# Performance work log

Hardware: AMD Instinct MI355X
Metric: run time of the kernel (lower is better)

## Reference

```python
import jax, jax.numpy as jnp
import numpy as np
import math

B, TD, TP, D, H = 16, 256, 1024, 512, 8
DH = D // H
G_MIN = 0.05
LN_EPS = 1e-5
SCALE = 1.0 / math.sqrt(DH)


def _ln(x, g, b):
    m = jnp.mean(x, axis=-1, keepdims=True)
    v = jnp.var(x, axis=-1, keepdims=True)
    return (x - m) * jax.lax.rsqrt(v + LN_EPS) * g + b


def _evi(x, w1, b1, w2, b2, k):
    # EvidentialHead: Linear -> SiLU -> Linear(d->4), NIG params -> gate
    h = jax.nn.silu(x @ w1 + b1)
    p = h @ w2 + b2  # (B,T,4)
    gamma, nu, alpha, beta = jnp.split(p, 4, axis=-1)
    nu = jax.nn.softplus(nu) + 1e-6
    alpha = jax.nn.softplus(alpha) + 1.0
    beta = jax.nn.softplus(beta) + 1e-6
    sigma2 = beta / (nu * (alpha - 1.0))  # (B,T,1)
    g = jnp.clip(jnp.exp(-k * sigma2[..., 0]), G_MIN, 1.0)  # (B,T)
    return g


def _xattn(Q, KV, log_bias, wq, bq, wk, bk, wv, bv, wo, bo, lng, lnb):
    # Q: (B,M,D), KV: (B,N,D), log_bias: (B,N) added to logits pre-softmax
    Bq, M, _ = Q.shape
    N = KV.shape[1]
    q = (Q @ wq + bq).reshape(Bq, M, H, DH)
    k_ = (KV @ wk + bk).reshape(Bq, N, H, DH)
    v = (KV @ wv + bv).reshape(Bq, N, H, DH)
    scores = jnp.einsum('bmhd,bnhd->bhmn', q, k_) * SCALE
    scores = scores + log_bias[:, None, None, :]
    attn = jax.nn.softmax(scores, axis=-1)
    out = jnp.einsum('bhmn,bnhd->bmhd', attn, v).reshape(Bq, M, D)
    out = out @ wo + bo
    return _ln(Q + out, lng, lnb)


def _ffn(x, w1, b1, w2, b2, lng, lnb):
    # Linear(d,4d) -> SiLU -> Linear(4d,d) -> LayerNorm (no residual)
    h = jax.nn.silu(x @ w1 + b1)
    return _ln(h @ w2 + b2, lng, lnb)


def setup_inputs() -> dict:
    key = jax.random.key(0)
    ks = iter(jax.random.split(key, 64))

    def w(shape, s=0.02):
        return s * jax.random.normal(next(ks), shape, jnp.float32)

    def attn_params(pfx):
        p = {}
        for nm in ('wq', 'wk', 'wv', 'wo'):
            p[pfx + '_' + nm] = w((D, D))
        for nm in ('bq', 'bk', 'bv', 'bo'):
            p[pfx + '_' + nm] = jnp.zeros((D,), jnp.float32)
        p[pfx + '_lng'] = jnp.ones((D,), jnp.float32)
        p[pfx + '_lnb'] = jnp.zeros((D,), jnp.float32)
        return p

    def ffn_params(pfx):
        return {pfx + '_w1': w((D, 4 * D)), pfx + '_b1': jnp.zeros((4 * D,), jnp.float32),
                pfx + '_w2': w((4 * D, D)), pfx + '_b2': jnp.zeros((D,), jnp.float32),
                pfx + '_lng': jnp.ones((D,), jnp.float32), pfx + '_lnb': jnp.zeros((D,), jnp.float32)}

    inp = {
        'Hd': jax.random.normal(next(ks), (B, TD, D), jnp.float32),
        'Hp': jax.random.normal(next(ks), (B, TP, D), jnp.float32),
        'k': 1,
        'evid_w1': w((D, D)), 'evid_b1': jnp.zeros((D,), jnp.float32),
        'evid_w2': w((D, 4)), 'evid_b2': jnp.zeros((4,), jnp.float32),
        'evip_w1': w((D, D)), 'evip_b1': jnp.zeros((D,), jnp.float32),
        'evip_w2': w((D, 4)), 'evip_b2': jnp.zeros((4,), jnp.float32),
    }
    inp.update(attn_params('p2d'))
    inp.update(attn_params('d2p'))
    inp.update(ffn_params('ffnd'))
    inp.update(ffn_params('ffnp'))
    return inp


def reference(Hd, Hp, k,
              evid_w1, evid_b1, evid_w2, evid_b2,
              evip_w1, evip_b1, evip_w2, evip_b2,
              p2d_wq, p2d_wk, p2d_wv, p2d_wo, p2d_bq, p2d_bk, p2d_bv, p2d_bo, p2d_lng, p2d_lnb,
              d2p_wq, d2p_wk, d2p_wv, d2p_wo, d2p_bq, d2p_bk, d2p_bv, d2p_bo, d2p_lng, d2p_lnb,
              ffnd_w1, ffnd_b1, ffnd_w2, ffnd_b2, ffnd_lng, ffnd_lnb,
              ffnp_w1, ffnp_b1, ffnp_w2, ffnp_b2, ffnp_lng, ffnp_lnb):
    gd = _evi(Hd, evid_w1, evid_b1, evid_w2, evid_b2, k)  # (B,TD)
    gp = _evi(Hp, evip_w1, evip_b1, evip_w2, evip_b2, k)  # (B,TP)
    Hp2 = _xattn(Hp, Hd, jnp.log(gd + 1e-12),
                 p2d_wq, p2d_bq, p2d_wk, p2d_bk, p2d_wv, p2d_bv, p2d_wo, p2d_bo, p2d_lng, p2d_lnb)
    Hd2 = _xattn(Hd, Hp, jnp.log(gp + 1e-12),
                 d2p_wq, d2p_bq, d2p_wk, d2p_bk, d2p_wv, d2p_bv, d2p_wo, d2p_bo, d2p_lng, d2p_lnb)
    Hd_out = _ffn(Hd2, ffnd_w1, ffnd_b1, ffnd_w2, ffnd_b2, ffnd_lng, ffnd_lnb)
    Hp_out = _ffn(Hp2, ffnp_w1, ffnp_b1, ffnp_w2, ffnp_b2, ffnp_lng, ffnp_lnb)
    return (Hd_out, Hp_out, gd, gp)
```

## Files before the change

kernel.cpp:

```cpp
#include <hip/hip_runtime.h>
#include <stdint.h>
#include <math.h>

typedef unsigned short u16;
typedef __attribute__((ext_vector_type(8))) short bf16x8;
typedef __attribute__((ext_vector_type(8))) short short8;
typedef __attribute__((ext_vector_type(4))) float f32x4;
typedef __attribute__((ext_vector_type(4))) unsigned short u16x4;

#define NB 16
#define TDr 256
#define TPr 1024
#define DM 512
#define NH 8
#define DHEAD 64

__device__ __forceinline__ float us2f(u16 u) {
  union { float f; unsigned int i; } x; x.i = ((unsigned int)u) << 16; return x.f;
}
__device__ __forceinline__ u16 f2us(float f) {
  union { float fl; unsigned int i; } x; x.fl = f;
  unsigned int u = x.i;
  return (u16)((u + 0x7fffu + ((u >> 16) & 1u)) >> 16);
}

__global__ __launch_bounds__(64) void detect_kernel(const u16* __restrict__ raw,
                                                    int* __restrict__ flag)
{
  const int lane = threadIdx.x;
  float mx = 0.f;
  for (int i = lane; i < 256; i += 64) {
    float v = us2f(raw[i]);
    v = fabsf(v);
    if (isfinite(v)) mx = fmaxf(mx, v); else mx = 1e30f;
  }
#pragma unroll
  for (int o = 32; o; o >>= 1) mx = fmaxf(mx, __shfl_xor(mx, o));
  if (lane == 0) flag[0] = (mx > 1e10f) ? 1 : 0;
}

struct CvtDesc { const void* src; unsigned long dst_off; int n; };
struct CvtTable { CvtDesc d[42]; };

__global__ __launch_bounds__(256) void cvt_kernel(CvtTable t, u16* __restrict__ base,
                                                  const int* __restrict__ flag)
{
  const CvtDesc d = t.d[blockIdx.y];
  u16* dst = base + d.dst_off;
  const int isf32 = flag[0];
  const int stride = gridDim.x * 256;
  const int tid0 = blockIdx.x * 256 + threadIdx.x;
  if (d.n >= 8) {
    const int n8 = d.n >> 3;
    if (isf32) {
      const float* s = (const float*)d.src;
      for (int i = tid0; i < n8; i += stride) {
        f32x4 a = *(const f32x4*)&s[i * 8];
        f32x4 b = *(const f32x4*)&s[i * 8 + 4];
        short8 o;
        o[0]=(short)f2us(a[0]); o[1]=(short)f2us(a[1]); o[2]=(short)f2us(a[2]); o[3]=(short)f2us(a[3]);
        o[4]=(short)f2us(b[0]); o[5]=(short)f2us(b[1]); o[6]=(short)f2us(b[2]); o[7]=(short)f2us(b[3]);
        *(short8*)&dst[i * 8] = o;
      }
    } else {
      const short8* s = (const short8*)d.src;
      for (int i = tid0; i < n8; i += stride) *(short8*)&dst[i * 8] = s[i];
    }
  } else {
    if (isf32) {
      const float* s = (const float*)d.src;
      for (int i = tid0; i < d.n; i += stride) dst[i] = f2us(s[i]);
    } else {
      const u16* s = (const u16*)d.src;
      for (int i = tid0; i < d.n; i += stride) dst[i] = s[i];
    }
  }
}

template<int BM, int BN>
__device__ __forceinline__ void gemm_core(
    const u16* __restrict__ Ab, const u16* __restrict__ Bb,
    int K, int tid, f32x4 (&acc)[BM/32][BN/32])
{
  constexpr int BK = 32;
  constexpr int FM = BM / 32;
  constexpr int FN = BN / 32;
  constexpr int LPT = (BM * BK / 8 + BN * BK / 8) / 256;
  __shared__ __align__(16) u16 As[2][BM * BK];
  __shared__ __align__(16) u16 Bs[2][BN * BK];

  const int lane = tid & 63;
  const int wm = (tid >> 6) >> 1;
  const int wn = (tid >> 6) & 1;

#pragma unroll
  for (int i = 0; i < FM; ++i)
#pragma unroll
    for (int j = 0; j < FN; ++j)
      acc[i][j] = (f32x4){0.f, 0.f, 0.f, 0.f};

  auto stage = [&](int buf, int k0) {
#pragma unroll
    for (int c = tid; c < BM * BK / 8; c += 256) {
      const int r  = c >> 2;
      const int kk = (c & 3) << 3;
      __builtin_amdgcn_global_load_lds(
          (const __attribute__((address_space(1))) uint32_t*)(Ab + (long)r * K + k0 + kk),
          (__attribute__((address_space(3))) uint32_t*)(&As[buf][c * 8]), 16, 0, 0);
    }
#pragma unroll
    for (int c = tid; c < BN * BK / 8; c += 256) {
      const int r  = c >> 2;
      const int kk = (c & 3) << 3;
      __builtin_amdgcn_global_load_lds(
          (const __attribute__((address_space(1))) uint32_t*)(Bb + (long)r * K + k0 + kk),
          (__attribute__((address_space(3))) uint32_t*)(&Bs[buf][c * 8]), 16, 0, 0);
    }
  };

  const int nt = K / BK;
  stage(0, 0);
  if (nt > 1) stage(1, BK);

  for (int t = 0; t < nt; ++t) {
    if (t + 1 < nt) {
      if constexpr (LPT == 4) asm volatile("s_waitcnt vmcnt(4)" ::: "memory");
      else                    asm volatile("s_waitcnt vmcnt(3)" ::: "memory");
    } else {
      asm volatile("s_waitcnt vmcnt(0)" ::: "memory");
    }
    asm volatile("s_barrier" ::: "memory");
    __builtin_amdgcn_sched_barrier(0);

    const int cur = t & 1;
    bf16x8 af[FM], bfv[FN];
#pragma unroll
    for (int i = 0; i < FM; ++i)
      af[i] = *(const bf16x8*)&As[cur][(wm * (BM/2) + i*16 + (lane & 15)) * BK + ((lane >> 4) << 3)];
#pragma unroll
    for (int j = 0; j < FN; ++j)
      bfv[j] = *(const bf16x8*)&Bs[cur][(wn * (BN/2) + j*16 + (lane & 15)) * BK + ((lane >> 4) << 3)];
#pragma unroll
    for (int i = 0; i < FM; ++i)
#pragma unroll
      for (int j = 0; j < FN; ++j)
        acc[i][j] = __builtin_amdgcn_mfma_f32_16x16x32_bf16(af[i], bfv[j], acc[i][j], 0, 0, 0);

    __builtin_amdgcn_sched_barrier(0);
    asm volatile("s_barrier" ::: "memory");
    __builtin_amdgcn_sched_barrier(0);
    if (t + 2 < nt) stage(cur, (t + 2) * BK);
  }
}

struct ProjSet {
  const u16 *A, *W, *bE, *bQ, *bK, *bV;
  u16 *H, *Q, *Kc, *VT;
  int ntokLog, mtiles;
};

__global__ __launch_bounds__(256, 4) void proj_pair(ProjSet s0, ProjSet s1)
{
  const ProjSet S = blockIdx.z ? s1 : s0;
  if ((int)blockIdx.x >= S.mtiles) return;
  const int tid = threadIdx.x;
  const int lane = tid & 63;
  const int wm = (tid >> 6) >> 1, wn = (tid >> 6) & 1;
  const int r16 = lane & 15, rr4 = (lane >> 4) << 2;
  const long row0 = (long)blockIdx.x * 128;
  const long col0 = (long)blockIdx.y * 128;

  f32x4 acc[4][4];
  gemm_core<128,128>(S.A + row0 * 512, S.W + col0 * 512, 512, tid, acc);

  const int range = (int)(col0 >> 9);
  const u16* bp = range == 0 ? S.bE : range == 1 ? S.bQ : range == 2 ? S.bK : S.bV;
  u16* dst = range == 0 ? S.H : range == 1 ? S.Q : S.Kc;
  const int ntok = 1 << S.ntokLog;

#pragma unroll
  for (int i = 0; i < 4; ++i) {
    const long gr0 = row0 + wm*64 + i*16 + rr4;
#pragma unroll
    for (int j = 0; j < 4; ++j) {
      const int cr = (int)(col0 & 511) + wn*64 + j*16 + r16;
      const float badd = us2f(bp[cr]);
      if (range == 3) {
        const long b = gr0 >> S.ntokLog;
        const long t0 = gr0 & (ntok - 1);
        u16x4 pk;
#pragma unroll
        for (int r = 0; r < 4; ++r) pk[r] = f2us(acc[i][j][r] + badd);
        *(u16x4*)&S.VT[((long)b * 512 + cr) * ntok + t0] = pk;
      } else if (range == 0) {
#pragma unroll
        for (int r = 0; r < 4; ++r) {
          float v = acc[i][j][r] + badd;
          v = v / (1.f + __expf(-v));
          dst[(gr0 + r) * 512 + cr] = f2us(v);
        }
      } else {
#pragma unroll
        for (int r = 0; r < 4; ++r)
          dst[(gr0 + r) * 512 + cr] = f2us(acc[i][j][r] + badd);
      }
    }
  }
}

struct Gm { const u16* A; const u16* Bt; const u16* bias; u16* C; int mtiles; };

template<int SILU>
__global__ __launch_bounds__(256, 4) void gemm_pair(Gm g0, Gm g1, int ldc, int K)
{
  const Gm G = blockIdx.z ? g1 : g0;
  if ((int)blockIdx.x >= G.mtiles) return;
  const int tid = threadIdx.x;
  const int lane = tid & 63;
  const int wm = (tid >> 6) >> 1, wn = (tid >> 6) & 1;
  const int r16 = lane & 15, rr4 = (lane >> 4) << 2;
  const long row0 = (long)blockIdx.x * 128;
  const long col0 = (long)blockIdx.y * 128;

  f32x4 acc[4][4];
  gemm_core<128,128>(G.A + row0 * (long)K, G.Bt + col0 * (long)K, K, tid, acc);

#pragma unroll
  for (int i = 0; i < 4; ++i) {
    const long gr0 = row0 + wm*64 + i*16 + rr4;
#pragma unroll
    for (int j = 0; j < 4; ++j) {
      const long gc = col0 + wn*64 + j*16 + r16;
      const float badd = us2f(G.bias[gc]);
#pragma unroll
      for (int r = 0; r < 4; ++r) {
        float v = acc[i][j][r] + badd;
        if (SILU) v = v / (1.f + __expf(-v));
        G.C[(gr0 + r) * (long)ldc + gc] = f2us(v);
      }
    }
  }
}

template<int NKV, int RPW>
__global__ __launch_bounds__(256) void attn_fused(
    const u16* __restrict__ Qp, const u16* __restrict__ Kp,
    const u16* __restrict__ Vt, const float* __restrict__ lb,
    u16* __restrict__ Aout, int M)
{
  constexpr int NC = NKV >> 7;
  constexpr int FI = RPW / 16;
  constexpr int NS = 4 * FI;
  constexpr int QT = 4 * RPW;
  constexpr int PLD = 136;
  __shared__ __align__(16) u16 Ps[4][RPW][PLD];

  const int tid  = threadIdx.x;
  const int lane = tid & 63;
  const int w    = tid >> 6;
  const int bh = blockIdx.y;
  const int b = bh >> 3, h = bh & 7;
  const long q0 = (long)blockIdx.x * QT;

  const u16* Qb = Qp + ((long)b * M + q0) * DM + h * DHEAD;
  const u16* Kb = Kp + (long)b * NKV * DM + h * DHEAD;
  const u16* Vb = Vt + ((long)b * DM + h * DHEAD) * NKV;
  const float* lbb = lb + (long)b * NKV;

  const int r16 = lane & 15;
  const int k8  = (lane >> 4) << 3;
  const int rr4 = (lane >> 4) << 2;
  const float SCALE = 0.125f;

  bf16x8 qa[FI][2];
#pragma unroll
  for (int i = 0; i < FI; ++i)
#pragma unroll
    for (int kc = 0; kc < 2; ++kc)
      qa[i][kc] = *(const bf16x8*)&Qb[(long)(w*RPW + i*16 + r16) * DM + kc*32 + k8];

  f32x4 acc_o[FI][4];
#pragma unroll
  for (int i = 0; i < FI; ++i)
#pragma unroll
    for (int jo = 0; jo < 4; ++jo)
      acc_o[i][jo] = (f32x4){0.f, 0.f, 0.f, 0.f};
  float mrow[NS], lrow[NS];
#pragma unroll
  for (int s = 0; s < NS; ++s) { mrow[s] = -1e30f; lrow[s] = 0.f; }

#pragma unroll
  for (int c = 0; c < NC; ++c) {
    const int t0 = c * 128;
    f32x4 acc_s[FI][8];
#pragma unroll
    for (int i = 0; i < FI; ++i)
#pragma unroll
      for (int j = 0; j < 8; ++j)
        acc_s[i][j] = (f32x4){0.f, 0.f, 0.f, 0.f};
#pragma unroll
    for (int j = 0; j < 8; ++j) {
      const long trow = t0 + j*16 + r16;
      bf16x8 kb0 = *(const bf16x8*)&Kb[trow * DM + k8];
      bf16x8 kb1 = *(const bf16x8*)&Kb[trow * DM + 32 + k8];
#pragma unroll
      for (int i = 0; i < FI; ++i) {
        acc_s[i][j] = __builtin_amdgcn_mfma_f32_16x16x32_bf16(qa[i][0], kb0, acc_s[i][j], 0, 0, 0);
        acc_s[i][j] = __builtin_amdgcn_mfma_f32_16x16x32_bf16(qa[i][1], kb1, acc_s[i][j], 0, 0, 0);
      }
    }

    float lbv[8];
#pragma unroll
    for (int j = 0; j < 8; ++j) lbv[j] = lbb[t0 + j*16 + r16];
    float pm[NS];
#pragma unroll
    for (int s = 0; s < NS; ++s) pm[s] = -1e30f;
#pragma unroll
    for (int i = 0; i < FI; ++i)
#pragma unroll
      for (int j = 0; j < 8; ++j)
#pragma unroll
        for (int r = 0; r < 4; ++r) {
          float v = acc_s[i][j][r] * SCALE + lbv[j];
          acc_s[i][j][r] = v;
          pm[i*4 + r] = fmaxf(pm[i*4 + r], v);
        }
#pragma unroll
    for (int s = 0; s < NS; ++s) {
#pragma unroll
      for (int o = 1; o < 16; o <<= 1) pm[s] = fmaxf(pm[s], __shfl_xor(pm[s], o));
    }
    float sc[NS];
#pragma unroll
    for (int s = 0; s < NS; ++s) {
      const float mn = fmaxf(mrow[s], pm[s]);
      sc[s] = __expf(mrow[s] - mn);
      mrow[s] = mn;
      lrow[s] *= sc[s];
    }
#pragma unroll
    for (int i = 0; i < FI; ++i)
#pragma unroll
      for (int jo = 0; jo < 4; ++jo)
#pragma unroll
        for (int r = 0; r < 4; ++r)
          acc_o[i][jo][r] *= sc[i*4 + r];

    float ls[NS];
#pragma unroll
    for (int s = 0; s < NS; ++s) ls[s] = 0.f;
#pragma unroll
    for (int i = 0; i < FI; ++i)
#pragma unroll
      for (int j = 0; j < 8; ++j)
#pragma unroll
        for (int r = 0; r < 4; ++r) {
          const float p = __expf(acc_s[i][j][r] - mrow[i*4 + r]);
          ls[i*4 + r] += p;
          Ps[w][i*16 + rr4 + r][j*16 + r16] = f2us(p);
        }
#pragma unroll
    for (int s = 0; s < NS; ++s) {
#pragma unroll
      for (int o = 1; o < 16; o <<= 1) ls[s] += __shfl_xor(ls[s], o);
      lrow[s] += ls[s];
    }

    asm volatile("s_waitcnt lgkmcnt(0)" ::: "memory");
    __builtin_amdgcn_sched_barrier(0);

#pragma unroll
    for (int kc = 0; kc < 4; ++kc) {
      bf16x8 pa[FI];
#pragma unroll
      for (int i = 0; i < FI; ++i)
        pa[i] = *(const bf16x8*)&Ps[w][i*16 + r16][kc*32 + k8];
#pragma unroll
      for (int jo = 0; jo < 4; ++jo) {
        bf16x8 vb = *(const bf16x8*)&Vb[(long)(jo*16 + r16) * NKV + t0 + kc*32 + k8];
#pragma unroll
        for (int i = 0; i < FI; ++i)
          acc_o[i][jo] = __builtin_amdgcn_mfma_f32_16x16x32_bf16(pa[i], vb, acc_o[i][jo], 0, 0, 0);
      }
    }
    __builtin_amdgcn_sched_barrier(0);
  }

  float linv[NS];
#pragma unroll
  for (int s = 0; s < NS; ++s) linv[s] = 1.f / lrow[s];
  u16* Ob = Aout + ((long)b * M + q0) * DM + h * DHEAD;
#pragma unroll
  for (int i = 0; i < FI; ++i)
#pragma unroll
    for (int jo = 0; jo < 4; ++jo)
#pragma unroll
      for (int r = 0; r < 4; ++r) {
        const long row = w*RPW + i*16 + rr4 + r;
        Ob[row * DM + jo*16 + r16] = f2us(acc_o[i][jo][r] * linv[i*4 + r]);
      }
}

struct TTab { const u16* in; u16* out; int R, C; };
struct TTable { TTab d[14]; };

__global__ __launch_bounds__(256) void transpose_all(TTable tt)
{
  const TTab d = tt.d[blockIdx.z];
  __shared__ u16 t[32][33];
  const int tx = threadIdx.x & 31, ty = threadIdx.x >> 5;
  for (int r0 = blockIdx.y * 32; r0 < d.R; r0 += gridDim.y * 32) {
    for (int c0 = blockIdx.x * 32; c0 < d.C; c0 += gridDim.x * 32) {
#pragma unroll
      for (int i = 0; i < 4; ++i)
        t[ty + 8*i][tx] = d.in[(long)(r0 + ty + 8*i) * d.C + c0 + tx];
      __syncthreads();
#pragma unroll
      for (int i = 0; i < 4; ++i)
        d.out[(long)(c0 + ty + 8*i) * d.R + r0 + tx] = t[tx][ty + 8*i];
      __syncthreads();
    }
  }
}

struct LnR { const u16* X; const u16* P; const u16* g; const u16* b; u16* out; int rows; };

__global__ __launch_bounds__(256) void ln_res_pair(LnR a0, LnR a1)
{
  const LnR A = blockIdx.z ? a1 : a0;
  const int row = blockIdx.x * 4 + (threadIdx.x >> 6);
  if (row >= A.rows) return;
  const int lane = threadIdx.x & 63;
  const u16* pr = A.P + (long)row * DM;
  const u16* xr = A.X + (long)row * DM;
  float v[8], s = 0.f, s2 = 0.f;
#pragma unroll
  for (int i = 0; i < 8; ++i) {
    const int jx = i * 64 + lane;
    float t = us2f(pr[jx]) + us2f(xr[jx]);
    v[i] = t; s += t; s2 += t * t;
  }
#pragma unroll
  for (int o = 32; o; o >>= 1) { s += __shfl_xor(s, o); s2 += __shfl_xor(s2, o); }
  const float mean = s * (1.f / DM);
  const float var  = s2 * (1.f / DM) - mean * mean;
  const float rstd = rsqrtf(fmaxf(var, 0.f) + 1e-5f);
#pragma unroll
  for (int i = 0; i < 8; ++i) {
    const int jx = i * 64 + lane;
    A.out[(long)row * DM + jx] = f2us((v[i] - mean) * rstd * us2f(A.g[jx]) + us2f(A.b[jx]));
  }
}

struct LnF { const u16* P; const u16* g; const u16* b; long oofs; int rows; };

__global__ __launch_bounds__(256) void ln_final_pair(LnF a0, LnF a1,
                                                     void* __restrict__ outb,
                                                     const int* __restrict__ flag)
{
  const LnF A = blockIdx.z ? a1 : a0;
  const int row = blockIdx.x * 4 + (threadIdx.x >> 6);
  if (row >= A.rows) return;
  const int lane = threadIdx.x & 63;
  const u16* pr = A.P + (long)row * DM;
  float v[8], s = 0.f, s2 = 0.f;
#pragma unroll
  for (int i = 0; i < 8; ++i) {
    const int jx = i * 64 + lane;
    float t = us2f(pr[jx]);
    v[i] = t; s += t; s2 += t * t;
  }
#pragma unroll
  for (int o = 32; o; o >>= 1) { s += __shfl_xor(s, o); s2 += __shfl_xor(s2, o); }
  const float mean = s * (1.f / DM);
  const float var  = s2 * (1.f / DM) - mean * mean;
  const float rstd = rsqrtf(fmaxf(var, 0.f) + 1e-5f);
  const int isf32 = flag[0];
#pragma unroll
  for (int i = 0; i < 8; ++i) {
    const int jx = i * 64 + lane;
    const float ov = (v[i] - mean) * rstd * us2f(A.g[jx]) + us2f(A.b[jx]);
    if (isf32) ((float*)outb)[A.oofs + (long)row * DM + jx] = ov;
    else       ((u16*)outb)[A.oofs + (long)row * DM + jx] = f2us(ov);
  }
}

struct Gt { const u16* H; const u16* W2; const u16* b2; long oofs; float* lb; int rows; };

__global__ __launch_bounds__(256) void gate_pair(Gt a0, Gt a1,
                                                 const int* __restrict__ kptr,
                                                 void* __restrict__ outb,
                                                 const int* __restrict__ flag)
{
  const Gt A = blockIdx.z ? a1 : a0;
  const int row = blockIdx.x * 4 + (threadIdx.x >> 6);
  if (row >= A.rows) return;
  const int lane = threadIdx.x & 63;
  const u16* hr = A.H + (long)row * DM;
  float p1 = 0.f, p2 = 0.f, p3 = 0.f;
#pragma unroll
  for (int i = 0; i < 8; ++i) {
    const int idx = i * 64 + lane;
    const float hv = us2f(hr[idx]);
    const u16x4 w = *(const u16x4*)&A.W2[idx * 4];
    p1 += hv * us2f(w[1]);
    p2 += hv * us2f(w[2]); p3 += hv * us2f(w[3]);
  }
#pragma unroll
  for (int o = 32; o; o >>= 1) {
    p1 += __shfl_xor(p1, o);
    p2 += __shfl_xor(p2, o); p3 += __shfl_xor(p3, o);
  }
  if (lane == 0) {
    const float nu = p1 + us2f(A.b2[1]);
    const float al = p2 + us2f(A.b2[2]);
    const float be = p3 + us2f(A.b2[3]);
    auto sp = [](float x) { return x > 20.f ? x : log1pf(expf(x)); };
    const float spn = sp(nu) + 1e-6f;
    const float spa = sp(al);
    const float spb = sp(be) + 1e-6f;
    const float sig = spb / (spn * spa);
    const float kk = (float)kptr[0];
    float gg = expf(-kk * sig);
    gg = fminf(fmaxf(gg, 0.05f), 1.f);
    if (flag[0]) ((float*)outb)[A.oofs + row] = gg;
    else         ((u16*)outb)[A.oofs + row] = f2us(gg);
    A.lb[row] = logf(gg + 1e-12f);
  }
}

extern "C" void kernel_launch(void* const* d_in, const int* in_sizes, int n_in,
                              void* d_out, int out_size, void* d_ws, size_t ws_size,
                              hipStream_t stream)
{
  const int* kptr = (const int*)d_in[2];

  uint8_t* base = (uint8_t*)d_ws;
  size_t off = 0;
  auto take = [&](size_t bytes) -> void* {
    void* p = base + off;
    off += (bytes + 255) & ~(size_t)255;
    return p;
  };
  int* FLAG = (int*)take(256);

  const int sizes[42] = {
    2097152, 8388608,
    262144, 512, 2048, 4,
    262144, 512, 2048, 4,
    262144,262144,262144,262144, 512,512,512,512, 512,512,
    262144,262144,262144,262144, 512,512,512,512, 512,512,
    1048576, 2048, 1048576, 512, 512, 512,
    1048576, 2048, 1048576, 512, 512, 512
  };
  u16* canon[42];
  u16* cbase = (u16*)take(17319944ul * 2 + 256);
  {
    unsigned long coff = 0;
    for (int i = 0; i < 42; ++i) {
      canon[i] = cbase + coff;
      coff += (unsigned long)((sizes[i] + 7) & ~7);
    }
  }
  const u16 *HdC = canon[0], *HpC = canon[1];
  const u16 *evid_w1 = canon[2], *evid_b1 = canon[3], *evid_w2 = canon[4], *evid_b2 = canon[5];
  const u16 *evip_w1 = canon[6], *evip_b1 = canon[7], *evip_w2 = canon[8], *evip_b2 = canon[9];
  const u16 *p2d_wq = canon[10], *p2d_wk = canon[11], *p2d_wv = canon[12], *p2d_wo = canon[13];
  const u16 *p2d_bq = canon[14], *p2d_bk = canon[15], *p2d_bv = canon[16], *p2d_bo = canon[17];
  const u16 *p2d_lng = canon[18], *p2d_lnb = canon[19];
  const u16 *d2p_wq = canon[20], *d2p_wk = canon[21], *d2p_wv = canon[22], *d2p_wo = canon[23];
  const u16 *d2p_bq = canon[24], *d2p_bk = canon[25], *d2p_bv = canon[26], *d2p_bo = canon[27];
  const u16 *d2p_lng = canon[28], *d2p_lnb = canon[29];
  const u16 *ffnd_w1 = canon[30], *ffnd_b1 = canon[31], *ffnd_w2 = canon[32], *ffnd_b2 = canon[33];
  const u16 *ffnd_lng = canon[34], *ffnd_lnb = canon[35];
  const u16 *ffnp_w1 = canon[36], *ffnp_b1 = canon[37], *ffnp_w2 = canon[38], *ffnp_b2 = canon[39];
  const u16 *ffnp_lng = canon[40], *ffnp_lnb = canon[41];

  u16* HpW = (u16*)take((size_t)2048*512*2);
  u16* HdW = (u16*)take((size_t)2048*512*2);
  u16* woT_p = (u16*)take((size_t)512*512*2);
  u16* woT_d = (u16*)take((size_t)512*512*2);
  u16* ffnp_w1T = (u16*)take((size_t)2048*512*2);
  u16* ffnp_w2T = (u16*)take((size_t)512*2048*2);
  u16* ffnd_w1T = (u16*)take((size_t)2048*512*2);
  u16* ffnd_w2T = (u16*)take((size_t)512*2048*2);

  u16* HBUF_p = (u16*)take((size_t)16384*512*2);
  u16* HBUF_d = (u16*)take((size_t)4096*512*2);
  u16* QBUF_p = (u16*)take((size_t)16384*512*2);
  u16* QBUF_d = (u16*)take((size_t)4096*512*2);
  u16* KBUF_p = (u16*)take((size_t)16384*512*2);
  u16* KBUF_d = (u16*)take((size_t)4096*512*2);
  u16* VT_p   = (u16*)take((size_t)16384*512*2);
  u16* VT_d   = (u16*)take((size_t)4096*512*2);
  u16* ABUF_p = (u16*)take((size_t)16384*512*2);
  u16* ABUF_d = (u16*)take((size_t)4096*512*2);
  u16* HP2  = (u16*)take((size_t)16384*512*2);
  u16* HD2  = (u16*)take((size_t)4096*512*2);
  float* LBD  = (float*)take((size_t)NB*TDr*4);
  float* LBP  = (float*)take((size_t)NB*TPr*4);
  if (off > ws_size) return;

  u16* PBUF_p = HBUF_p;
  u16* PBUF_d = HBUF_d;
  u16* SBUF_p = QBUF_p;
  u16* SBUF_d = SBUF_p + (size_t)16384*2048;

  const long O_HD = 0;
  const long O_HP = 2097152;
  const long O_GD = 10485760;
  const long O_GP = 10489856;

  detect_kernel<<<dim3(1), 64, 0, stream>>>((const u16*)d_in[0], FLAG);
  CvtTable tbl;
  {
    int ii = 0;
    for (int i = 0; i < 43; ++i) {
      if (i == 2) continue;
      tbl.d[ii].src = d_in[i];
      tbl.d[ii].dst_off = (unsigned long)(canon[ii] - cbase);
      tbl.d[ii].n = sizes[ii];
      ++ii;
    }
  }
  cvt_kernel<<<dim3(64, 42), 256, 0, stream>>>(tbl, cbase, FLAG);

  TTable tt;
  {
    const TTab tts[14] = {
      {evip_w1, HpW + 0*512*512, 512, 512},
      {p2d_wq,  HpW + 1*512*512, 512, 512},
      {d2p_wk,  HpW + 2*512*512, 512, 512},
      {d2p_wv,  HpW + 3*512*512, 512, 512},
      {evid_w1, HdW + 0*512*512, 512, 512},
      {d2p_wq,  HdW + 1*512*512, 512, 512},
      {p2d_wk,  HdW + 2*512*512, 512, 512},
      {p2d_wv,  HdW + 3*512*512, 512, 512},
      {p2d_wo, woT_p, 512, 512}, {d2p_wo, woT_d, 512, 512},
      {ffnp_w1, ffnp_w1T, 512, 2048}, {ffnp_w2, ffnp_w2T, 2048, 512},
      {ffnd_w1, ffnd_w1T, 512, 2048}, {ffnd_w2, ffnd_w2T, 2048, 512},
    };
    for (int i = 0; i < 14; ++i) tt.d[i] = tts[i];
  }
  transpose_all<<<dim3(16, 16, 14), 256, 0, stream>>>(tt);

  ProjSet sp{HpC, HpW, evip_b1, p2d_bq, d2p_bk, d2p_bv,
             HBUF_p, QBUF_p, KBUF_p, VT_p, 10, 128};
  ProjSet sd{HdC, HdW, evid_b1, d2p_bq, p2d_bk, p2d_bv,
             HBUF_d, QBUF_d, KBUF_d, VT_d, 8, 32};
  proj_pair<<<dim3(128, 16, 2), 256, 0, stream>>>(sp, sd);

  Gt gp{HBUF_p, evip_w2, evip_b2, O_GP, LBP, 16384};
  Gt gd{HBUF_d, evid_w2, evid_b2, O_GD, LBD, 4096};
  gate_pair<<<dim3(4096, 1, 2), 256, 0, stream>>>(gp, gd, kptr, d_out, FLAG);

  attn_fused<TDr,32><<<dim3(TPr/128, NB*NH), 256, 0, stream>>>(
      QBUF_p, KBUF_d, VT_d, LBD, ABUF_p, TPr);
  attn_fused<TPr,16><<<dim3(TDr/64, NB*NH), 256, 0, stream>>>(
      QBUF_d, KBUF_p, VT_p, LBP, ABUF_d, TDr);

  Gm wp{ABUF_p, woT_p, p2d_bo, PBUF_p, 128};
  Gm wd{ABUF_d, woT_d, d2p_bo, PBUF_d, 32};
  gemm_pair<0><<<dim3(128, 4, 2), 256, 0, stream>>>(wp, wd, 512, 512);

  LnR lp{HpC, PBUF_p, p2d_lng, p2d_lnb, HP2, 16384};
  LnR ld{HdC, PBUF_d, d2p_lng, d2p_lnb, HD2, 4096};
  ln_res_pair<<<dim3(4096, 1, 2), 256, 0, stream>>>(lp, ld);

  Gm f1p{HP2, ffnp_w1T, ffnp_b1, SBUF_p, 128};
  Gm f1d{HD2, ffnd_w1T, ffnd_b1, SBUF_d, 32};
  gemm_pair<1><<<dim3(128, 16, 2), 256, 0, stream>>>(f1p, f1d, 2048, 512);

  Gm f2p{SBUF_p, ffnp_w2T, ffnp_b2, PBUF_p, 128};
  Gm f2d{SBUF_d, ffnd_w2T, ffnd_b2, PBUF_d, 32};
  gemm_pair<0><<<dim3(128, 4, 2), 256, 0, stream>>>(f2p, f2d, 512, 2048);

  LnF fp{PBUF_p, ffnp_lng, ffnp_lnb, O_HP, 16384};
  LnF fd{PBUF_d, ffnd_lng, ffnd_lnb, O_HD, 4096};
  ln_final_pair<<<dim3(4096, 1, 2), 256, 0, stream>>>(fp, fd, d_out, FLAG);
}
```

Measured before the change: 438.2 us.

## Triple-buffer GEMM pipeline, fuse attention launches, transpose weights directly from inputs

The GEMM core moves from double to triple buffering of LDS tiles, with deeper vmcnt waits, and occupancy hints for the projection and pair GEMMs drop from 4 to 3. The two attention kernels become one launch that picks the direction from blockIdx.z. Weight matrices are no longer converted to canonical bf16 first; the transpose kernel reads the raw inputs and converts on the fly, removing one copy pass. Together these aim to hide global-load latency better and cut launch and copy overhead, at the cost of more LDS per block and possibly lower occupancy.

```diff
diff --git a/kernel.cpp b/kernel.cpp
--- a/kernel.cpp
+++ b/kernel.cpp
@@ -40,7 +40,7 @@
 }
 
 struct CvtDesc { const void* src; unsigned long dst_off; int n; };
-struct CvtTable { CvtDesc d[42]; };
+struct CvtTable { CvtDesc d[28]; };
 
 __global__ __launch_bounds__(256) void cvt_kernel(CvtTable t, u16* __restrict__ base,
                                                   const int* __restrict__ flag)
@@ -77,6 +77,32 @@
   }
 }
 
+struct TTab { const void* in; u16* out; int R, C; };
+struct TTable { TTab d[14]; };
+
+__global__ __launch_bounds__(256) void transpose_all(TTable tt, const int* __restrict__ flag)
+{
+  const TTab d = tt.d[blockIdx.z];
+  const int isf32 = flag[0];
+  __shared__ u16 t[32][33];
+  const int tx = threadIdx.x & 31, ty = threadIdx.x >> 5;
+  for (int r0 = blockIdx.y * 32; r0 < d.R; r0 += gridDim.y * 32) {
+    for (int c0 = blockIdx.x * 32; c0 < d.C; c0 += gridDim.x * 32) {
+#pragma unroll
+      for (int i = 0; i < 4; ++i) {
+        const long idx = (long)(r0 + ty + 8*i) * d.C + c0 + tx;
+        t[ty + 8*i][tx] = isf32 ? f2us(((const float*)d.in)[idx])
+                                : ((const u16*)d.in)[idx];
+      }
+      __syncthreads();
+#pragma unroll
+      for (int i = 0; i < 4; ++i)
+        d.out[(long)(c0 + ty + 8*i) * d.R + r0 + tx] = t[tx][ty + 8*i];
+      __syncthreads();
+    }
+  }
+}
+
 template<int BM, int BN>
 __device__ __forceinline__ void gemm_core(
     const u16* __restrict__ Ab, const u16* __restrict__ Bb,
@@ -85,9 +111,8 @@
   constexpr int BK = 32;
   constexpr int FM = BM / 32;
   constexpr int FN = BN / 32;
-  constexpr int LPT = (BM * BK / 8 + BN * BK / 8) / 256;
-  __shared__ __align__(16) u16 As[2][BM * BK];
-  __shared__ __align__(16) u16 Bs[2][BN * BK];
+  __shared__ __align__(16) u16 As[3][BM * BK];
+  __shared__ __align__(16) u16 Bs[3][BN * BK];
 
   const int lane = tid & 63;
   const int wm = (tid >> 6) >> 1;
@@ -121,18 +146,16 @@
   const int nt = K / BK;
   stage(0, 0);
   if (nt > 1) stage(1, BK);
+  if (nt > 2) stage(2, 2 * BK);
 
   for (int t = 0; t < nt; ++t) {
-    if (t + 1 < nt) {
-      if constexpr (LPT == 4) asm volatile("s_waitcnt vmcnt(4)" ::: "memory");
-      else                    asm volatile("s_waitcnt vmcnt(3)" ::: "memory");
-    } else {
-      asm volatile("s_waitcnt vmcnt(0)" ::: "memory");
-    }
+    if (t + 2 < nt)      asm volatile("s_waitcnt vmcnt(8)" ::: "memory");
+    else if (t + 1 < nt) asm volatile("s_waitcnt vmcnt(4)" ::: "memory");
+    else                 asm volatile("s_waitcnt vmcnt(0)" ::: "memory");
     asm volatile("s_barrier" ::: "memory");
     __builtin_amdgcn_sched_barrier(0);
 
-    const int cur = t & 1;
+    const int cur = t % 3;
     bf16x8 af[FM], bfv[FN];
 #pragma unroll
     for (int i = 0; i < FM; ++i)
@@ -149,7 +172,7 @@
     __builtin_amdgcn_sched_barrier(0);
     asm volatile("s_barrier" ::: "memory");
     __builtin_amdgcn_sched_barrier(0);
-    if (t + 2 < nt) stage(cur, (t + 2) * BK);
+    if (t + 3 < nt) stage(cur, (t + 3) * BK);
   }
 }
 
@@ -159,7 +182,7 @@
   int ntokLog, mtiles;
 };
 
-__global__ __launch_bounds__(256, 4) void proj_pair(ProjSet s0, ProjSet s1)
+__global__ __launch_bounds__(256, 3) void proj_pair(ProjSet s0, ProjSet s1)
 {
   const ProjSet S = blockIdx.z ? s1 : s0;
   if ((int)blockIdx.x >= S.mtiles) return;
@@ -211,7 +234,7 @@
 struct Gm { const u16* A; const u16* Bt; const u16* bias; u16* C; int mtiles; };
 
 template<int SILU>
-__global__ __launch_bounds__(256, 4) void gemm_pair(Gm g0, Gm g1, int ldc, int K)
+__global__ __launch_bounds__(256, 3) void gemm_pair(Gm g0, Gm g1, int ldc, int K)
 {
   const Gm G = blockIdx.z ? g1 : g0;
   if ((int)blockIdx.x >= G.mtiles) return;
@@ -243,17 +266,16 @@
 }
 
 template<int NKV, int RPW>
-__global__ __launch_bounds__(256) void attn_fused(
+__device__ __forceinline__ void attn_body(
     const u16* __restrict__ Qp, const u16* __restrict__ Kp,
     const u16* __restrict__ Vt, const float* __restrict__ lb,
-    u16* __restrict__ Aout, int M)
+    u16* __restrict__ Aout, int M, u16* __restrict__ Ps)
 {
   constexpr int NC = NKV >> 7;
   constexpr int FI = RPW / 16;
   constexpr int NS = 4 * FI;
   constexpr int QT = 4 * RPW;
   constexpr int PLD = 136;
-  __shared__ __align__(16) u16 Ps[4][RPW][PLD];
 
   const int tid  = threadIdx.x;
   const int lane = tid & 63;
@@ -271,6 +293,7 @@
   const int k8  = (lane >> 4) << 3;
   const int rr4 = (lane >> 4) << 2;
   const float SCALE = 0.125f;
+  u16* Pw = Ps + (w * RPW) * PLD;
 
   bf16x8 qa[FI][2];
 #pragma unroll
@@ -358,7 +381,7 @@
         for (int r = 0; r < 4; ++r) {
           const float p = __expf(acc_s[i][j][r] - mrow[i*4 + r]);
           ls[i*4 + r] += p;
-          Ps[w][i*16 + rr4 + r][j*16 + r16] = f2us(p);
+          Pw[(i*16 + rr4 + r) * PLD + j*16 + r16] = f2us(p);
         }
 #pragma unroll
     for (int s = 0; s < NS; ++s) {
@@ -375,7 +398,7 @@
       bf16x8 pa[FI];
 #pragma unroll
       for (int i = 0; i < FI; ++i)
-        pa[i] = *(const bf16x8*)&Ps[w][i*16 + r16][kc*32 + k8];
+        pa[i] = *(const bf16x8*)&Pw[(i*16 + r16) * PLD + kc*32 + k8];
 #pragma unroll
       for (int jo = 0; jo < 4; ++jo) {
         bf16x8 vb = *(const bf16x8*)&Vb[(long)(jo*16 + r16) * NKV + t0 + kc*32 + k8];
@@ -402,25 +425,16 @@
       }
 }
 
-struct TTab { const u16* in; u16* out; int R, C; };
-struct TTable { TTab d[14]; };
-
-__global__ __launch_bounds__(256) void transpose_all(TTable tt)
-{
-  const TTab d = tt.d[blockIdx.z];
-  __shared__ u16 t[32][33];
-  const int tx = threadIdx.x & 31, ty = threadIdx.x >> 5;
-  for (int r0 = blockIdx.y * 32; r0 < d.R; r0 += gridDim.y * 32) {
-    for (int c0 = blockIdx.x * 32; c0 < d.C; c0 += gridDim.x * 32) {
-#pragma unroll
-      for (int i = 0; i < 4; ++i)
-        t[ty + 8*i][tx] = d.in[(long)(r0 + ty + 8*i) * d.C + c0 + tx];
-      __syncthreads();
-#pragma unroll
-      for (int i = 0; i < 4; ++i)
-        d.out[(long)(c0 + ty + 8*i) * d.R + r0 + tx] = t[tx][ty + 8*i];
-      __syncthreads();
-    }
+__global__ __launch_bounds__(256) void attn_both(
+    const u16* Qp0, const u16* Kp0, const u16* Vt0, const float* lb0, u16* Ao0,
+    const u16* Qp1, const u16* Kp1, const u16* Vt1, const float* lb1, u16* Ao1)
+{
+  __shared__ __align__(16) u16 Ps[4 * 32 * 136];
+  if (blockIdx.z == 0) {
+    attn_body<TDr, 32>(Qp0, Kp0, Vt0, lb0, Ao0, TPr, Ps);
+  } else {
+    if ((int)blockIdx.x >= TDr / 64) return;
+    attn_body<TPr, 16>(Qp1, Kp1, Vt1, lb1, Ao1, TDr, Ps);
   }
 }
 
@@ -564,17 +578,15 @@
     }
   }
   const u16 *HdC = canon[0], *HpC = canon[1];
-  const u16 *evid_w1 = canon[2], *evid_b1 = canon[3], *evid_w2 = canon[4], *evid_b2 = canon[5];
-  const u16 *evip_w1 = canon[6], *evip_b1 = canon[7], *evip_w2 = canon[8], *evip_b2 = canon[9];
-  const u16 *p2d_wq = canon[10], *p2d_wk = canon[11], *p2d_wv = canon[12], *p2d_wo = canon[13];
+  const u16 *evid_b1 = canon[3], *evid_w2 = canon[4], *evid_b2 = canon[5];
+  const u16 *evip_b1 = canon[7], *evip_w2 = canon[8], *evip_b2 = canon[9];
   const u16 *p2d_bq = canon[14], *p2d_bk = canon[15], *p2d_bv = canon[16], *p2d_bo = canon[17];
   const u16 *p2d_lng = canon[18], *p2d_lnb = canon[19];
-  const u16 *d2p_wq = canon[20], *d2p_wk = canon[21], *d2p_wv = canon[22], *d2p_wo = canon[23];
   const u16 *d2p_bq = canon[24], *d2p_bk = canon[25], *d2p_bv = canon[26], *d2p_bo = canon[27];
   const u16 *d2p_lng = canon[28], *d2p_lnb = canon[29];
-  const u16 *ffnd_w1 = canon[30], *ffnd_b1 = canon[31], *ffnd_w2 = canon[32], *ffnd_b2 = canon[33];
+  const u16 *ffnd_b1 = canon[31], *ffnd_b2 = canon[33];
   const u16 *ffnd_lng = canon[34], *ffnd_lnb = canon[35];
-  const u16 *ffnp_w1 = canon[36], *ffnp_b1 = canon[37], *ffnp_w2 = canon[38], *ffnp_b2 = canon[39];
+  const u16 *ffnp_b1 = canon[37], *ffnp_b2 = canon[39];
   const u16 *ffnp_lng = canon[40], *ffnp_lnb = canon[41];
 
   u16* HpW = (u16*)take((size_t)2048*512*2);
@@ -613,37 +625,44 @@
   const long O_GP = 10489856;
 
   detect_kernel<<<dim3(1), 64, 0, stream>>>((const u16*)d_in[0], FLAG);
+
   CvtTable tbl;
   {
+    const int skip[14] = {2,6,10,11,12,13,20,21,22,23,30,32,36,38};
     int ii = 0;
-    for (int i = 0; i < 43; ++i) {
-      if (i == 2) continue;
-      tbl.d[ii].src = d_in[i];
-      tbl.d[ii].dst_off = (unsigned long)(canon[ii] - cbase);
-      tbl.d[ii].n = sizes[ii];
+    for (int ci = 0; ci < 42; ++ci) {
+      bool sk = false;
+      for (int s = 0; s < 14; ++s) if (skip[s] == ci) { sk = true; break; }
+      if (sk) continue;
+      tbl.d[ii].src = d_in[ci < 2 ? ci : ci + 1];
+      tbl.d[ii].dst_off = (unsigned long)(canon[ci] - cbase);
+      tbl.d[ii].n = sizes[ci];
       ++ii;
     }
   }
-  cvt_kernel<<<dim3(64, 42), 256, 0, stream>>>(tbl, cbase, FLAG);
+  cvt_kernel<<<dim3(64, 28), 256, 0, stream>>>(tbl, cbase, FLAG);
 
   TTable tt;
   {
     const TTab tts[14] = {
-      {evip_w1, HpW + 0*512*512, 512, 512},
-      {p2d_wq,  HpW + 1*512*512, 512, 512},
-      {d2p_wk,  HpW + 2*512*512, 512, 512},
-      {d2p_wv,  HpW + 3*512*512, 512, 512},
-      {evid_w1, HdW + 0*512*512, 512, 512},
-      {d2p_wq,  HdW + 1*512*512, 512, 512},
-      {p2d_wk,  HdW + 2*512*512, 512, 512},
-      {p2d_wv,  HdW + 3*512*512, 512, 512},
-      {p2d_wo, woT_p, 512, 512}, {d2p_wo, woT_d, 512, 512},
-      {ffnp_w1, ffnp_w1T, 512, 2048}, {ffnp_w2, ffnp_w2T, 2048, 512},
-      {ffnd_w1, ffnd_w1T, 512, 2048}, {ffnd_w2, ffnd_w2T, 2048, 512},
+      {d_in[7],  HpW + 0*512*512, 512, 512},
+      {d_in[11], HpW + 1*512*512, 512, 512},
+      {d_in[22], HpW + 2*512*512, 512, 512},
+      {d_in[23], HpW + 3*512*512, 512, 512},
+      {d_in[3],  HdW + 0*512*512, 512, 512},
+      {d_in[21], HdW + 1*512*512, 512, 512},
+      {d_in[12], HdW + 2*512*512, 512, 512},
+      {d_in[13], HdW + 3*512*512, 512, 512},
+      {d_in[14], woT_p, 512, 512},
+      {d_in[24], woT_d, 512, 512},
+      {d_in[37], ffnp_w1T, 512, 2048},
+      {d_in[39], ffnp_w2T, 2048, 512},
+      {d_in[31], ffnd_w1T, 512, 2048},
+      {d_in[33], ffnd_w2T, 2048, 512},
     };
     for (int i = 0; i < 14; ++i) tt.d[i] = tts[i];
   }
-  transpose_all<<<dim3(16, 16, 14), 256, 0, stream>>>(tt);
+  transpose_all<<<dim3(16, 16, 14), 256, 0, stream>>>(tt, FLAG);
 
   ProjSet sp{HpC, HpW, evip_b1, p2d_bq, d2p_bk, d2p_bv,
              HBUF_p, QBUF_p, KBUF_p, VT_p, 10, 128};
@@ -655,10 +674,9 @@
   Gt gd{HBUF_d, evid_w2, evid_b2, O_GD, LBD, 4096};
   gate_pair<<<dim3(4096, 1, 2), 256, 0, stream>>>(gp, gd, kptr, d_out, FLAG);
 
-  attn_fused<TDr,32><<<dim3(TPr/128, NB*NH), 256, 0, stream>>>(
-      QBUF_p, KBUF_d, VT_d, LBD, ABUF_p, TPr);
-  attn_fused<TPr,16><<<dim3(TDr/64, NB*NH), 256, 0, stream>>>(
-      QBUF_d, KBUF_p, VT_p, LBP, ABUF_d, TDr);
+  attn_both<<<dim3(TPr/128, NB*NH, 2), 256, 0, stream>>>(
+      QBUF_p, KBUF_d, VT_d, LBD, ABUF_p,
+      QBUF_d, KBUF_p, VT_p, LBP, ABUF_d);
 
   Gm wp{ABUF_p, woT_p, p2d_bo, PBUF_p, 128};
   Gm wd{ABUF_d, woT_d, d2p_bo, PBUF_d, 32};
```

After: 480.4 us. +9.6%, slower.
